# Kernel tuning notes

Hardware: AMD Instinct MI355X
Metric: run time of the kernel (lower is better)

Reference implementation:

```python
import jax, jax.numpy as jnp
import numpy as np

B, S, D, H = 4, 2048, 1024, 16
HD = D // H  # head_dim = 64


def setup_inputs() -> dict:
    key = jax.random.key(0)
    ks = jax.random.split(key, 8)
    scale = 1.0 / np.sqrt(D)
    return {
        "hidden_states": jax.random.normal(ks[0], (B, S, D), dtype=jnp.float32),
        "attention_mask": jnp.zeros((B, 1, 1, S), dtype=jnp.float32),
        "Wq": jax.random.normal(ks[1], (D, D), dtype=jnp.float32) * scale,
        "bq": jnp.zeros((D,), dtype=jnp.float32),
        "Wk": jax.random.normal(ks[2], (D, D), dtype=jnp.float32) * scale,
        "bk": jnp.zeros((D,), dtype=jnp.float32),
        "Wv": jax.random.normal(ks[3], (D, D), dtype=jnp.float32) * scale,
        "bv": jnp.zeros((D,), dtype=jnp.float32),
    }


def reference(hidden_states, attention_mask, Wq, bq, Wk, bk, Wv, bv):
    def split_heads(x):
        # [B,S,D] -> [B,H,S,HD]
        return x.reshape(B, S, H, HD).transpose(0, 2, 1, 3)

    q = split_heads(hidden_states @ Wq + bq)
    k = split_heads(hidden_states @ Wk + bk)
    v = split_heads(hidden_states @ Wv + bv)

    # [B,H,S,S]
    scores = jnp.einsum("bhqd,bhkd->bhqk", q, k) / jnp.sqrt(jnp.float32(HD))
    scores = scores + attention_mask  # additive mask, broadcasts [B,1,1,S]
    probs = jax.nn.softmax(scores, axis=-1)

    ctx = jnp.einsum("bhqk,bhkd->bhqd", probs, v)  # [B,H,S,HD]
    return ctx.transpose(0, 2, 1, 3).reshape(B, S, D)
```

## Files before the change

kernel.cpp:

```cpp
#include <hip/hip_runtime.h>
#include <hip/hip_bf16.h>
#include <stdint.h>

typedef __attribute__((ext_vector_type(4))) float f32x4;
typedef __attribute__((ext_vector_type(16))) float f32x16;
typedef __attribute__((ext_vector_type(8))) short bf16x8;
typedef __attribute__((ext_vector_type(4))) int int4v;
typedef __attribute__((ext_vector_type(8))) unsigned short u16x8;
typedef unsigned int u32;

static __device__ __forceinline__ unsigned short f2bf(float f) {
    union { float f; unsigned u; } v; v.f = f;
    unsigned r = v.u + 0x7FFF + ((v.u >> 16) & 1);
    return (unsigned short)(r >> 16);
}

static __device__ __forceinline__ u32 cvtpk(float lo, float hi) {
    u32 r;
    asm("v_cvt_pk_bf16_f32 %0, %1, %2" : "=v"(r) : "v"(lo), "v"(hi));
    return r;
}

static __device__ __forceinline__ void pl32swap_u(u32& a, u32& b) {
    asm("v_permlane32_swap_b32 %0, %1" : "+v"(a), "+v"(b));
}

static __device__ __forceinline__ void gload16(const void* g, void* lds) {
    __builtin_amdgcn_global_load_lds((const __attribute__((address_space(1))) void*)g,
                                     (__attribute__((address_space(3))) void*)lds,
                                     16, 0, 0);
}

__global__ __launch_bounds__(256) void cvt_x_kernel(const float* __restrict__ x,
                                                    unsigned short* __restrict__ xb) {
    int i = (blockIdx.x * 256 + threadIdx.x) * 4;
    float4 v = *(const float4*)(x + i);
    ushort4 o = make_ushort4(f2bf(v.x), f2bf(v.y), f2bf(v.z), f2bf(v.w));
    *(ushort4*)(xb + i) = o;
}

__global__ __launch_bounds__(256) void cvt_w_kernel(const float* __restrict__ Wq,
                                                    const float* __restrict__ Wk,
                                                    const float* __restrict__ Wv,
                                                    unsigned short* __restrict__ Wt3) {
    const float* W = (blockIdx.z == 0) ? Wq : ((blockIdx.z == 1) ? Wk : Wv);
    unsigned short* out = Wt3 + (size_t)blockIdx.z * 1024 * 1024;
    __shared__ unsigned short t[64][68];
    int k0 = blockIdx.x * 64, n0 = blockIdx.y * 64;
    int tid = threadIdx.x;
#pragma unroll
    for (int i = 0; i < 4; i++) {
        int c = i * 256 + tid;
        int row = c >> 4, cb = c & 15;
        float4 v = *(const float4*)(W + (size_t)(k0 + row) * 1024 + n0 + cb * 4);
        ushort4 o = make_ushort4(f2bf(v.x), f2bf(v.y), f2bf(v.z), f2bf(v.w));
        *(ushort4*)(&t[row][cb * 4]) = o;
    }
    __syncthreads();
#pragma unroll
    for (int i = 0; i < 2; i++) {
        int c = i * 256 + tid;
        int n = c >> 3, kc = c & 7;
        u16x8 tmp;
#pragma unroll
        for (int j = 0; j < 8; j++) tmp[j] = t[kc * 8 + j][n];
        *(u16x8*)(&out[(size_t)(n0 + n) * 1024 + k0 + kc * 8]) = tmp;
    }
}

__global__ __launch_bounds__(256) void mask_reorder_kernel(const float* __restrict__ mask,
                                                           float* __restrict__ maskr) {
    int o = blockIdx.x * 256 + threadIdx.x;
    int reg = o & 15, kvb = (o >> 4) & 1, hi2 = (o >> 5) & 1, kt = (o >> 6) & 31, bb = o >> 11;
    int kv = kt * 64 + kvb * 32 + (reg & 3) + 8 * (reg >> 2) + 4 * hi2;
    maskr[o] = 8.0f * mask[bb * 2048 + kv];
}

__global__ __launch_bounds__(256) void qkv_gemm_kernel(
    const unsigned short* __restrict__ Xb,
    const unsigned short* __restrict__ Wt3,
    const float* __restrict__ bq, const float* __restrict__ bk, const float* __restrict__ bv,
    unsigned short* __restrict__ Qo, unsigned short* __restrict__ Ko,
    unsigned short* __restrict__ Vt)
{
    int z = blockIdx.z;
    const unsigned short* Wt = Wt3 + (size_t)z * 1048576;
    const float* bias = (z == 0) ? bq : ((z == 1) ? bk : bv);
    int m0 = blockIdx.x * 128, n0 = blockIdx.y * 128;

    __shared__ __align__(16) unsigned short As[128 * 64];
    __shared__ __align__(16) unsigned short Bs[128 * 64];

    int tid = threadIdx.x, lane = tid & 63, wave = tid >> 6;
    int wm = wave >> 1, wn = wave & 1;
    int lr = lane & 15, lg = lane >> 4;

    const int chunkrow = lane >> 3, colp = (lane & 7) * 8;
    const unsigned short* aBase = Xb + (size_t)(m0 + wave * 32 + chunkrow) * 1024 + colp;
    const unsigned short* bBase = Wt + (size_t)(n0 + wave * 32 + chunkrow) * 1024 + colp;
    char* lA = (char*)As + wave * 4096;
    char* lB = (char*)Bs + wave * 4096;

    f32x4 acc[4][4] = {};

    for (int kt = 0; kt < 16; kt++) {
        int kbase = kt * 64;
#pragma unroll
        for (int c = 0; c < 4; c++) {
            gload16(aBase + kbase + c * 8192, lA + c * 1024);
            gload16(bBase + kbase + c * 8192, lB + c * 1024);
        }
        __syncthreads();
#pragma unroll
        for (int kk = 0; kk < 2; kk++) {
            bf16x8 a[4], bb[4];
#pragma unroll
            for (int mi = 0; mi < 4; mi++)
                a[mi] = *(const bf16x8*)((char*)As + (wm * 64 + mi * 16 + lr) * 128 + kk * 64 + lg * 16);
#pragma unroll
            for (int ni = 0; ni < 4; ni++)
                bb[ni] = *(const bf16x8*)((char*)Bs + (wn * 64 + ni * 16 + lr) * 128 + kk * 64 + lg * 16);
#pragma unroll
            for (int mi = 0; mi < 4; mi++)
#pragma unroll
                for (int ni = 0; ni < 4; ni++)
                    acc[mi][ni] = __builtin_amdgcn_mfma_f32_16x16x32_bf16(a[mi], bb[ni], acc[mi][ni], 0, 0, 0);
        }
        __syncthreads();
    }

    if (z < 2) {
        unsigned short* out = (z == 0) ? Qo : Ko;
#pragma unroll
        for (int ni = 0; ni < 4; ni++) {
            int n = n0 + wn * 64 + ni * 16 + lr;
            float bsv = bias[n];
#pragma unroll
            for (int mi = 0; mi < 4; mi++) {
                int mrow = m0 + wm * 64 + mi * 16 + lg * 4;
#pragma unroll
                for (int r = 0; r < 4; r++)
                    out[(size_t)(mrow + r) * 1024 + n] = f2bf(acc[mi][ni][r] + bsv);
            }
        }
    } else {
#pragma unroll
        for (int ni = 0; ni < 4; ni++) {
            int n = n0 + wn * 64 + ni * 16 + lr;
            float bsv = bias[n];
            int h = n >> 6, hd = n & 63;
#pragma unroll
            for (int mi = 0; mi < 4; mi++) {
                int mrow = m0 + wm * 64 + mi * 16 + lg * 4;
                int b = mrow >> 11, s = mrow & 2047;
                ushort4 pk = make_ushort4(f2bf(acc[mi][ni][0] + bsv),
                                          f2bf(acc[mi][ni][1] + bsv),
                                          f2bf(acc[mi][ni][2] + bsv),
                                          f2bf(acc[mi][ni][3] + bsv));
                *(ushort4*)(&Vt[((size_t)(b * 16 + h) * 64 + hd) * 2048 + s]) = pk;
            }
        }
    }
}

__global__ __launch_bounds__(256) void attn_kernel(
    const unsigned short* __restrict__ Q,
    const unsigned short* __restrict__ K,
    const unsigned short* __restrict__ Vt,
    const float* __restrict__ maskr,
    float* __restrict__ out)
{
    __shared__ __align__(16) char smem[33280];
    const int tid = threadIdx.x, lane = tid & 63, w = tid >> 6;
    const int ln31 = lane & 31, hi = lane >> 5;
    const int bh = blockIdx.y, b = bh >> 4, h = bh & 15;
    const int q0 = blockIdx.x * 128 + w * 32;
    const int swz = (ln31 & 7) << 4;
    const float c1 = 0.18033688011112042f;
    const float DTHR = 44.361f;

    const unsigned short* Qrow = Q + (size_t)(b * 2048 + q0 + ln31) * 1024 + h * 64;
    bf16x8 aq[4];
#pragma unroll
    for (int ds = 0; ds < 4; ds++) aq[ds] = *(const bf16x8*)(Qrow + ds * 16 + hi * 8);

    const unsigned short* Kbp = K + (size_t)b * 2048 * 1024 + h * 64;
    const unsigned short* Vbp = Vt + (size_t)bh * 64 * 2048;

    const int r0 = tid >> 3, cb = tid & 7;
    const int woff = r0 * 128 + ((cb * 16) ^ ((r0 & 7) << 4));

    const unsigned short* kp = Kbp + (size_t)r0 * 1024 + cb * 8;
    const unsigned short* vp = Vbp + (size_t)r0 * 2048 + cb * 8;
    const float* mp = maskr + (size_t)b * 2048 + tid * 4;

    f32x16 oacc0 = {}, oacc1 = {};
    float mrun = 8.0f;
    float lrun = 0.f;

    int4v kr0, kr1, vr0, vr1, mr = {};
    kr0 = *(const int4v*)kp; kr1 = *(const int4v*)(kp + 32 * 1024);
    vr0 = *(const int4v*)vp; vr1 = *(const int4v*)(vp + 32 * 2048);
    if (tid < 16) mr = *(const int4v*)mp;
    kp += 65536; vp += 64; mp += 64;
    *(int4v*)(smem + woff) = kr0;
    *(int4v*)(smem + 32 * 128 + woff) = kr1;
    *(int4v*)(smem + 16384 + woff) = vr0;
    *(int4v*)(smem + 16384 + 32 * 128 + woff) = vr1;
    if (tid < 16) *(int4v*)(smem + 32768 + tid * 16) = mr;
    kr0 = *(const int4v*)kp; kr1 = *(const int4v*)(kp + 32 * 1024);
    vr0 = *(const int4v*)vp; vr1 = *(const int4v*)(vp + 32 * 2048);
    if (tid < 16) mr = *(const int4v*)mp;
    kp += 65536; vp += 64; mp += 64;
    __syncthreads();

#pragma unroll 2
    for (int kt = 0; kt < 32; kt++) {
        const int cur = kt & 1;
        const char* KsL = smem + cur * 8192 + ln31 * 128;
        const char* VsL = KsL + 16384;
        const f32x4* mpl = (const f32x4*)(smem + 32768 + cur * 256 + hi * 128);

        f32x16 st0, st1;
        {
            f32x4 a0 = mpl[0], a1 = mpl[1], a2 = mpl[2], a3 = mpl[3];
            f32x4 a4 = mpl[4], a5 = mpl[5], a6 = mpl[6], a7 = mpl[7];
#pragma unroll
            for (int j = 0; j < 4; j++) {
                st0[j] = a0[j]; st0[4 + j] = a1[j]; st0[8 + j] = a2[j]; st0[12 + j] = a3[j];
                st1[j] = a4[j]; st1[4 + j] = a5[j]; st1[8 + j] = a6[j]; st1[12 + j] = a7[j];
            }
        }

        __builtin_amdgcn_s_setprio(1);
#pragma unroll
        for (int ds = 0; ds < 4; ds++) {
            const int co = (ds * 32 + hi * 16) ^ swz;
            bf16x8 ka0 = *(const bf16x8*)(KsL + co);
            bf16x8 ka1 = *(const bf16x8*)(KsL + 4096 + co);
            st0 = __builtin_amdgcn_mfma_f32_32x32x16_bf16(ka0, aq[ds], st0, 0, 0, 0);
            st1 = __builtin_amdgcn_mfma_f32_32x32x16_bf16(ka1, aq[ds], st1, 0, 0, 0);
        }
        __builtin_amdgcn_s_setprio(0);

        float m8[8];
#pragma unroll
        for (int j = 0; j < 8; j++)
            m8[j] = fmaxf(fmaxf(st0[j], st0[j + 8]), fmaxf(st1[j], st1[j + 8]));
        float mx = fmaxf(fmaxf(fmaxf(m8[0], m8[1]), fmaxf(m8[2], m8[3])),
                         fmaxf(fmaxf(m8[4], m8[5]), fmaxf(m8[6], m8[7])));

        if (__any(mx > mrun + DTHR)) {
            float mo = fmaxf(mx, __shfl_xor(mx, 32));
            const float mnew = fmaxf(mrun, mo);
            const float al = __builtin_amdgcn_exp2f((mrun - mnew) * c1);
            mrun = mnew;
            lrun *= al;
#pragma unroll
            for (int j = 0; j < 16; j++) { oacc0[j] *= al; oacc1[j] *= al; }
        }
        const float mc = mrun * c1;

        float s16[16];
#pragma unroll
        for (int j = 0; j < 16; j++) {
            float v0 = __builtin_amdgcn_exp2f(__builtin_fmaf(st0[j], c1, -mc));
            float v1 = __builtin_amdgcn_exp2f(__builtin_fmaf(st1[j], c1, -mc));
            st0[j] = v0; st1[j] = v1; s16[j] = v0 + v1;
        }
#pragma unroll
        for (int stp = 8; stp > 0; stp >>= 1)
#pragma unroll
            for (int j = 0; j < 8; j++) if (j < stp) s16[j] += s16[j + stp];
        lrun += s16[0];

        __builtin_amdgcn_s_setprio(1);
#pragma unroll
        for (int s = 0; s < 4; s++) {
            const f32x16& pp = (s & 2) ? st1 : st0;
            const int rA = (s & 1) * 8, rB = rA + 4;
            u32 w0 = cvtpk(pp[rA + 0], pp[rA + 1]);
            u32 w1 = cvtpk(pp[rA + 2], pp[rA + 3]);
            u32 w2 = cvtpk(pp[rB + 0], pp[rB + 1]);
            u32 w3 = cvtpk(pp[rB + 2], pp[rB + 3]);
            pl32swap_u(w0, w2);
            pl32swap_u(w1, w3);
            union { u32 u[4]; bf16x8 v; } pb;
            pb.u[0] = w0; pb.u[1] = w1; pb.u[2] = w2; pb.u[3] = w3;
            const int co = (s * 32 + hi * 16) ^ swz;
            bf16x8 va0 = *(const bf16x8*)(VsL + co);
            bf16x8 va1 = *(const bf16x8*)(VsL + 4096 + co);
            oacc0 = __builtin_amdgcn_mfma_f32_32x32x16_bf16(va0, pb.v, oacc0, 0, 0, 0);
            oacc1 = __builtin_amdgcn_mfma_f32_32x32x16_bf16(va1, pb.v, oacc1, 0, 0, 0);
        }
        __builtin_amdgcn_s_setprio(0);

        if (kt < 31) {
            char* base = smem + (cur ^ 1) * 8192;
            *(int4v*)(base + woff) = kr0;
            *(int4v*)(base + 32 * 128 + woff) = kr1;
            *(int4v*)(base + 16384 + woff) = vr0;
            *(int4v*)(base + 16384 + 32 * 128 + woff) = vr1;
            if (tid < 16) *(int4v*)(smem + 32768 + (cur ^ 1) * 256 + tid * 16) = mr;
            if (kt < 30) {
                kr0 = *(const int4v*)kp; kr1 = *(const int4v*)(kp + 32 * 1024);
                vr0 = *(const int4v*)vp; vr1 = *(const int4v*)(vp + 32 * 2048);
                if (tid < 16) mr = *(const int4v*)mp;
                kp += 65536; vp += 64; mp += 64;
            }
        }
        __syncthreads();
    }

    float lt = lrun + __shfl_xor(lrun, 32);
    const float rl = 1.0f / lt;
    float* lw = (float*)(smem + w * 4096);
    const int qp = lane >> 1, hb = (lane & 1) * 16;
#pragma unroll
    for (int p = 0; p < 2; p++) {
        const f32x16& oa = p ? oacc1 : oacc0;
#pragma unroll
        for (int r = 0; r < 16; r++) {
            int hd = (r & 3) + 8 * (r >> 2) + 4 * hi;
            lw[hd * 32 + ln31] = oa[r] * rl;
        }
        float* od = out + (size_t)(b * 2048 + q0 + qp) * 1024 + h * 64 + p * 32 + hb;
#pragma unroll
        for (int c = 0; c < 4; c++) {
            f32x4 o4;
#pragma unroll
            for (int j = 0; j < 4; j++) o4[j] = lw[(hb + c * 4 + j) * 32 + qp];
            *(f32x4*)(od + c * 4) = o4;
        }
        __syncthreads();
    }
}

extern "C" void kernel_launch(void* const* d_in, const int* in_sizes, int n_in,
                              void* d_out, int out_size, void* d_ws, size_t ws_size,
                              hipStream_t stream) {
    const float* hs   = (const float*)d_in[0];
    const float* mask = (const float*)d_in[1];
    const float* Wq   = (const float*)d_in[2];
    const float* bq   = (const float*)d_in[3];
    const float* Wk   = (const float*)d_in[4];
    const float* bk   = (const float*)d_in[5];
    const float* Wv   = (const float*)d_in[6];
    const float* bv   = (const float*)d_in[7];
    float* out = (float*)d_out;

    char* ws = (char*)d_ws;
    unsigned short* Xb  = (unsigned short*)ws;
    unsigned short* Wt3 = (unsigned short*)(ws + 16777216);
    unsigned short* Qb  = (unsigned short*)(ws + 16777216 + 6291456);
    unsigned short* Kb  = Qb + 8388608;
    unsigned short* Vt  = Kb + 8388608;
    float* maskr = (float*)(ws + 16777216 + 6291456 + 3 * 16777216);

    cvt_x_kernel<<<8192, 256, 0, stream>>>(hs, Xb);
    cvt_w_kernel<<<dim3(16, 16, 3), 256, 0, stream>>>(Wq, Wk, Wv, Wt3);
    mask_reorder_kernel<<<32, 256, 0, stream>>>(mask, maskr);
    qkv_gemm_kernel<<<dim3(64, 8, 3), 256, 0, stream>>>(Xb, Wt3, bq, bk, bv, Qb, Kb, Vt);
    attn_kernel<<<dim3(16, 64), 256, 0, stream>>>(Qb, Kb, Vt, maskr, out);
}
```

Measured before the change: 200.5 us.

## Process two 32-row query tiles per wave to reuse K/V fragments

Each wave now handles 64 query rows (two 32-row groups) instead of 32, so each block covers 256 queries and the grid halves to 8x64. K and V fragments read from shared memory are reused across both groups' MFMAs, halving LDS traffic and global K/V loads per query. The running max is shared across both groups while the row sums stay separate. The cost is roughly double the accumulator registers, which lowers occupancy, and only 512 blocks for the 256 CUs.

```diff
diff --git a/kernel.cpp b/kernel.cpp
--- a/kernel.cpp
+++ b/kernel.cpp
@@ -174,15 +174,19 @@
     const int tid = threadIdx.x, lane = tid & 63, w = tid >> 6;
     const int ln31 = lane & 31, hi = lane >> 5;
     const int bh = blockIdx.y, b = bh >> 4, h = bh & 15;
-    const int q0 = blockIdx.x * 128 + w * 32;
+    const int q0 = blockIdx.x * 256 + w * 64;
     const int swz = (ln31 & 7) << 4;
     const float c1 = 0.18033688011112042f;
     const float DTHR = 44.361f;
 
-    const unsigned short* Qrow = Q + (size_t)(b * 2048 + q0 + ln31) * 1024 + h * 64;
-    bf16x8 aq[4];
-#pragma unroll
-    for (int ds = 0; ds < 4; ds++) aq[ds] = *(const bf16x8*)(Qrow + ds * 16 + hi * 8);
+    const unsigned short* QrowA = Q + (size_t)(b * 2048 + q0 + ln31) * 1024 + h * 64;
+    const unsigned short* QrowB = QrowA + 32 * 1024;
+    bf16x8 aqA[4], aqB[4];
+#pragma unroll
+    for (int ds = 0; ds < 4; ds++) {
+        aqA[ds] = *(const bf16x8*)(QrowA + ds * 16 + hi * 8);
+        aqB[ds] = *(const bf16x8*)(QrowB + ds * 16 + hi * 8);
+    }
 
     const unsigned short* Kbp = K + (size_t)b * 2048 * 1024 + h * 64;
     const unsigned short* Vbp = Vt + (size_t)bh * 64 * 2048;
@@ -194,9 +198,9 @@
     const unsigned short* vp = Vbp + (size_t)r0 * 2048 + cb * 8;
     const float* mp = maskr + (size_t)b * 2048 + tid * 4;
 
-    f32x16 oacc0 = {}, oacc1 = {};
+    f32x16 oaccA0 = {}, oaccA1 = {}, oaccB0 = {}, oaccB1 = {};
     float mrun = 8.0f;
-    float lrun = 0.f;
+    float lrunA = 0.f, lrunB = 0.f;
 
     int4v kr0, kr1, vr0, vr1, mr = {};
     kr0 = *(const int4v*)kp; kr1 = *(const int4v*)(kp + 32 * 1024);
@@ -221,15 +225,16 @@
         const char* VsL = KsL + 16384;
         const f32x4* mpl = (const f32x4*)(smem + 32768 + cur * 256 + hi * 128);
 
-        f32x16 st0, st1;
+        f32x16 stA0, stA1, stB0, stB1;
         {
             f32x4 a0 = mpl[0], a1 = mpl[1], a2 = mpl[2], a3 = mpl[3];
             f32x4 a4 = mpl[4], a5 = mpl[5], a6 = mpl[6], a7 = mpl[7];
 #pragma unroll
             for (int j = 0; j < 4; j++) {
-                st0[j] = a0[j]; st0[4 + j] = a1[j]; st0[8 + j] = a2[j]; st0[12 + j] = a3[j];
-                st1[j] = a4[j]; st1[4 + j] = a5[j]; st1[8 + j] = a6[j]; st1[12 + j] = a7[j];
-            }
+                stA0[j] = a0[j]; stA0[4 + j] = a1[j]; stA0[8 + j] = a2[j]; stA0[12 + j] = a3[j];
+                stA1[j] = a4[j]; stA1[4 + j] = a5[j]; stA1[8 + j] = a6[j]; stA1[12 + j] = a7[j];
+            }
+            stB0 = stA0; stB1 = stA1;
         }
 
         __builtin_amdgcn_s_setprio(1);
@@ -238,15 +243,18 @@
             const int co = (ds * 32 + hi * 16) ^ swz;
             bf16x8 ka0 = *(const bf16x8*)(KsL + co);
             bf16x8 ka1 = *(const bf16x8*)(KsL + 4096 + co);
-            st0 = __builtin_amdgcn_mfma_f32_32x32x16_bf16(ka0, aq[ds], st0, 0, 0, 0);
-            st1 = __builtin_amdgcn_mfma_f32_32x32x16_bf16(ka1, aq[ds], st1, 0, 0, 0);
+            stA0 = __builtin_amdgcn_mfma_f32_32x32x16_bf16(ka0, aqA[ds], stA0, 0, 0, 0);
+            stB0 = __builtin_amdgcn_mfma_f32_32x32x16_bf16(ka0, aqB[ds], stB0, 0, 0, 0);
+            stA1 = __builtin_amdgcn_mfma_f32_32x32x16_bf16(ka1, aqA[ds], stA1, 0, 0, 0);
+            stB1 = __builtin_amdgcn_mfma_f32_32x32x16_bf16(ka1, aqB[ds], stB1, 0, 0, 0);
         }
         __builtin_amdgcn_s_setprio(0);
 
         float m8[8];
 #pragma unroll
         for (int j = 0; j < 8; j++)
-            m8[j] = fmaxf(fmaxf(st0[j], st0[j + 8]), fmaxf(st1[j], st1[j + 8]));
+            m8[j] = fmaxf(fmaxf(fmaxf(stA0[j], stA0[j + 8]), fmaxf(stA1[j], stA1[j + 8])),
+                          fmaxf(fmaxf(stB0[j], stB0[j + 8]), fmaxf(stB1[j], stB1[j + 8])));
         float mx = fmaxf(fmaxf(fmaxf(m8[0], m8[1]), fmaxf(m8[2], m8[3])),
                          fmaxf(fmaxf(m8[4], m8[5]), fmaxf(m8[6], m8[7])));
 
@@ -255,43 +263,58 @@
             const float mnew = fmaxf(mrun, mo);
             const float al = __builtin_amdgcn_exp2f((mrun - mnew) * c1);
             mrun = mnew;
-            lrun *= al;
-#pragma unroll
-            for (int j = 0; j < 16; j++) { oacc0[j] *= al; oacc1[j] *= al; }
+            lrunA *= al; lrunB *= al;
+#pragma unroll
+            for (int j = 0; j < 16; j++) {
+                oaccA0[j] *= al; oaccA1[j] *= al; oaccB0[j] *= al; oaccB1[j] *= al;
+            }
         }
         const float mc = mrun * c1;
 
-        float s16[16];
+        float sA[16], sB[16];
 #pragma unroll
         for (int j = 0; j < 16; j++) {
-            float v0 = __builtin_amdgcn_exp2f(__builtin_fmaf(st0[j], c1, -mc));
-            float v1 = __builtin_amdgcn_exp2f(__builtin_fmaf(st1[j], c1, -mc));
-            st0[j] = v0; st1[j] = v1; s16[j] = v0 + v1;
+            float a0 = __builtin_amdgcn_exp2f(__builtin_fmaf(stA0[j], c1, -mc));
+            float a1 = __builtin_amdgcn_exp2f(__builtin_fmaf(stA1[j], c1, -mc));
+            float b0 = __builtin_amdgcn_exp2f(__builtin_fmaf(stB0[j], c1, -mc));
+            float b1 = __builtin_amdgcn_exp2f(__builtin_fmaf(stB1[j], c1, -mc));
+            stA0[j] = a0; stA1[j] = a1; stB0[j] = b0; stB1[j] = b1;
+            sA[j] = a0 + a1; sB[j] = b0 + b1;
         }
 #pragma unroll
         for (int stp = 8; stp > 0; stp >>= 1)
 #pragma unroll
-            for (int j = 0; j < 8; j++) if (j < stp) s16[j] += s16[j + stp];
-        lrun += s16[0];
+            for (int j = 0; j < 8; j++) if (j < stp) { sA[j] += sA[j + stp]; sB[j] += sB[j + stp]; }
+        lrunA += sA[0]; lrunB += sB[0];
 
         __builtin_amdgcn_s_setprio(1);
 #pragma unroll
         for (int s = 0; s < 4; s++) {
-            const f32x16& pp = (s & 2) ? st1 : st0;
+            const f32x16& ppA = (s & 2) ? stA1 : stA0;
+            const f32x16& ppB = (s & 2) ? stB1 : stB0;
             const int rA = (s & 1) * 8, rB = rA + 4;
-            u32 w0 = cvtpk(pp[rA + 0], pp[rA + 1]);
-            u32 w1 = cvtpk(pp[rA + 2], pp[rA + 3]);
-            u32 w2 = cvtpk(pp[rB + 0], pp[rB + 1]);
-            u32 w3 = cvtpk(pp[rB + 2], pp[rB + 3]);
-            pl32swap_u(w0, w2);
-            pl32swap_u(w1, w3);
-            union { u32 u[4]; bf16x8 v; } pb;
-            pb.u[0] = w0; pb.u[1] = w1; pb.u[2] = w2; pb.u[3] = w3;
+            u32 a0 = cvtpk(ppA[rA + 0], ppA[rA + 1]);
+            u32 a1 = cvtpk(ppA[rA + 2], ppA[rA + 3]);
+            u32 a2 = cvtpk(ppA[rB + 0], ppA[rB + 1]);
+            u32 a3 = cvtpk(ppA[rB + 2], ppA[rB + 3]);
+            pl32swap_u(a0, a2);
+            pl32swap_u(a1, a3);
+            u32 b0 = cvtpk(ppB[rA + 0], ppB[rA + 1]);
+            u32 b1 = cvtpk(ppB[rA + 2], ppB[rA + 3]);
+            u32 b2 = cvtpk(ppB[rB + 0], ppB[rB + 1]);
+            u32 b3 = cvtpk(ppB[rB + 2], ppB[rB + 3]);
+            pl32swap_u(b0, b2);
+            pl32swap_u(b1, b3);
+            union { u32 u[4]; bf16x8 v; } pbA, pbB;
+            pbA.u[0] = a0; pbA.u[1] = a1; pbA.u[2] = a2; pbA.u[3] = a3;
+            pbB.u[0] = b0; pbB.u[1] = b1; pbB.u[2] = b2; pbB.u[3] = b3;
             const int co = (s * 32 + hi * 16) ^ swz;
             bf16x8 va0 = *(const bf16x8*)(VsL + co);
             bf16x8 va1 = *(const bf16x8*)(VsL + 4096 + co);
-            oacc0 = __builtin_amdgcn_mfma_f32_32x32x16_bf16(va0, pb.v, oacc0, 0, 0, 0);
-            oacc1 = __builtin_amdgcn_mfma_f32_32x32x16_bf16(va1, pb.v, oacc1, 0, 0, 0);
+            oaccA0 = __builtin_amdgcn_mfma_f32_32x32x16_bf16(va0, pbA.v, oaccA0, 0, 0, 0);
+            oaccB0 = __builtin_amdgcn_mfma_f32_32x32x16_bf16(va0, pbB.v, oaccB0, 0, 0, 0);
+            oaccA1 = __builtin_amdgcn_mfma_f32_32x32x16_bf16(va1, pbA.v, oaccA1, 0, 0, 0);
+            oaccB1 = __builtin_amdgcn_mfma_f32_32x32x16_bf16(va1, pbB.v, oaccB1, 0, 0, 0);
         }
         __builtin_amdgcn_s_setprio(0);
 
@@ -312,27 +335,32 @@
         __syncthreads();
     }
 
-    float lt = lrun + __shfl_xor(lrun, 32);
-    const float rl = 1.0f / lt;
+    float ltA = lrunA + __shfl_xor(lrunA, 32);
+    float ltB = lrunB + __shfl_xor(lrunB, 32);
+    const float rlA = 1.0f / ltA, rlB = 1.0f / ltB;
     float* lw = (float*)(smem + w * 4096);
     const int qp = lane >> 1, hb = (lane & 1) * 16;
 #pragma unroll
-    for (int p = 0; p < 2; p++) {
-        const f32x16& oa = p ? oacc1 : oacc0;
-#pragma unroll
-        for (int r = 0; r < 16; r++) {
-            int hd = (r & 3) + 8 * (r >> 2) + 4 * hi;
-            lw[hd * 32 + ln31] = oa[r] * rl;
-        }
-        float* od = out + (size_t)(b * 2048 + q0 + qp) * 1024 + h * 64 + p * 32 + hb;
-#pragma unroll
-        for (int c = 0; c < 4; c++) {
-            f32x4 o4;
-#pragma unroll
-            for (int j = 0; j < 4; j++) o4[j] = lw[(hb + c * 4 + j) * 32 + qp];
-            *(f32x4*)(od + c * 4) = o4;
-        }
-        __syncthreads();
+    for (int g = 0; g < 2; g++) {
+        const float rl = g ? rlB : rlA;
+#pragma unroll
+        for (int p = 0; p < 2; p++) {
+            const f32x16& oa = g ? (p ? oaccB1 : oaccB0) : (p ? oaccA1 : oaccA0);
+#pragma unroll
+            for (int r = 0; r < 16; r++) {
+                int hd = (r & 3) + 8 * (r >> 2) + 4 * hi;
+                lw[hd * 32 + ln31] = oa[r] * rl;
+            }
+            float* od = out + (size_t)(b * 2048 + q0 + g * 32 + qp) * 1024 + h * 64 + p * 32 + hb;
+#pragma unroll
+            for (int c = 0; c < 4; c++) {
+                f32x4 o4;
+#pragma unroll
+                for (int j = 0; j < 4; j++) o4[j] = lw[(hb + c * 4 + j) * 32 + qp];
+                *(f32x4*)(od + c * 4) = o4;
+            }
+            __syncthreads();
+        }
     }
 }
 
@@ -361,5 +389,5 @@
     cvt_w_kernel<<<dim3(16, 16, 3), 256, 0, stream>>>(Wq, Wk, Wv, Wt3);
     mask_reorder_kernel<<<32, 256, 0, stream>>>(mask, maskr);
     qkv_gemm_kernel<<<dim3(64, 8, 3), 256, 0, stream>>>(Xb, Wt3, bq, bk, bv, Qb, Kb, Vt);
-    attn_kernel<<<dim3(16, 64), 256, 0, stream>>>(Qb, Kb, Vt, maskr, out);
-}
+    attn_kernel<<<dim3(8, 64), 256, 0, stream>>>(Qb, Kb, Vt, maskr, out);
+}
```

After: 213.9 us. +6.7%, slower.

## Replace max-based online softmax rescale with post-exp sum check; move prefetch earlier

Applied to the files above, without the earlier changes.

Drops the per-tile row-max reduction before exponentiation. Exponentials are now computed against a running offset, and a rescale happens only when the exp sum exceeds a threshold: it divides by the max exp value and adds its log2 to the offset. The global-to-LDS stores and next-tile global loads move from after the PV MFMAs to right after the QK MFMAs, so memory traffic overlaps more with the softmax math. The change risks float overflow if scores jump sharply between tiles, since exp is now taken before any max check.

```diff
diff --git a/kernel.cpp b/kernel.cpp
--- a/kernel.cpp
+++ b/kernel.cpp
@@ -177,7 +177,6 @@
     const int q0 = blockIdx.x * 128 + w * 32;
     const int swz = (ln31 & 7) << 4;
     const float c1 = 0.18033688011112042f;
-    const float DTHR = 44.361f;
 
     const unsigned short* Qrow = Q + (size_t)(b * 2048 + q0 + ln31) * 1024 + h * 64;
     bf16x8 aq[4];
@@ -195,7 +194,7 @@
     const float* mp = maskr + (size_t)b * 2048 + tid * 4;
 
     f32x16 oacc0 = {}, oacc1 = {};
-    float mrun = 8.0f;
+    float mc = 8.0f * c1;
     float lrun = 0.f;
 
     int4v kr0, kr1, vr0, vr1, mr = {};
@@ -243,23 +242,20 @@
         }
         __builtin_amdgcn_s_setprio(0);
 
-        float m8[8];
-#pragma unroll
-        for (int j = 0; j < 8; j++)
-            m8[j] = fmaxf(fmaxf(st0[j], st0[j + 8]), fmaxf(st1[j], st1[j + 8]));
-        float mx = fmaxf(fmaxf(fmaxf(m8[0], m8[1]), fmaxf(m8[2], m8[3])),
-                         fmaxf(fmaxf(m8[4], m8[5]), fmaxf(m8[6], m8[7])));
-
-        if (__any(mx > mrun + DTHR)) {
-            float mo = fmaxf(mx, __shfl_xor(mx, 32));
-            const float mnew = fmaxf(mrun, mo);
-            const float al = __builtin_amdgcn_exp2f((mrun - mnew) * c1);
-            mrun = mnew;
-            lrun *= al;
-#pragma unroll
-            for (int j = 0; j < 16; j++) { oacc0[j] *= al; oacc1[j] *= al; }
-        }
-        const float mc = mrun * c1;
+        if (kt < 31) {
+            char* base = smem + (cur ^ 1) * 8192;
+            *(int4v*)(base + woff) = kr0;
+            *(int4v*)(base + 32 * 128 + woff) = kr1;
+            *(int4v*)(base + 16384 + woff) = vr0;
+            *(int4v*)(base + 16384 + 32 * 128 + woff) = vr1;
+            if (tid < 16) *(int4v*)(smem + 32768 + (cur ^ 1) * 256 + tid * 16) = mr;
+            if (kt < 30) {
+                kr0 = *(const int4v*)kp; kr1 = *(const int4v*)(kp + 32 * 1024);
+                vr0 = *(const int4v*)vp; vr1 = *(const int4v*)(vp + 32 * 2048);
+                if (tid < 16) mr = *(const int4v*)mp;
+                kp += 65536; vp += 64; mp += 64;
+            }
+        }
 
         float s16[16];
 #pragma unroll
@@ -272,6 +268,24 @@
         for (int stp = 8; stp > 0; stp >>= 1)
 #pragma unroll
             for (int j = 0; j < 8; j++) if (j < stp) s16[j] += s16[j + stp];
+
+        if (__any(s16[0] > 256.0f)) {
+            float me = st0[0];
+#pragma unroll
+            for (int j = 1; j < 16; j++) me = fmaxf(me, st0[j]);
+#pragma unroll
+            for (int j = 0; j < 16; j++) me = fmaxf(me, st1[j]);
+            me = fmaxf(me, __shfl_xor(me, 32));
+            me = fmaxf(me, 1.0f);
+            const float al = 1.0f / me;
+            mc += __log2f(me);
+            lrun *= al; s16[0] *= al;
+#pragma unroll
+            for (int j = 0; j < 16; j++) {
+                st0[j] *= al; st1[j] *= al;
+                oacc0[j] *= al; oacc1[j] *= al;
+            }
+        }
         lrun += s16[0];
 
         __builtin_amdgcn_s_setprio(1);
@@ -295,20 +309,6 @@
         }
         __builtin_amdgcn_s_setprio(0);
 
-        if (kt < 31) {
-            char* base = smem + (cur ^ 1) * 8192;
-            *(int4v*)(base + woff) = kr0;
-            *(int4v*)(base + 32 * 128 + woff) = kr1;
-            *(int4v*)(base + 16384 + woff) = vr0;
-            *(int4v*)(base + 16384 + 32 * 128 + woff) = vr1;
-            if (tid < 16) *(int4v*)(smem + 32768 + (cur ^ 1) * 256 + tid * 16) = mr;
-            if (kt < 30) {
-                kr0 = *(const int4v*)kp; kr1 = *(const int4v*)(kp + 32 * 1024);
-                vr0 = *(const int4v*)vp; vr1 = *(const int4v*)(vp + 32 * 2048);
-                if (tid < 16) mr = *(const int4v*)mp;
-                kp += 65536; vp += 64; mp += 64;
-            }
-        }
         __syncthreads();
     }
 
```

New measurement: 199.9 us. No clear change (-0.3%).
